# Kernel tuning notes

Measured on AMD Instinct MI355X. Metric: run time of the kernel, lower is better.

The kernel has to match this reference:

```python
import jax, jax.numpy as jnp
import numpy as np

B, H, W, C = 2, 64, 64, 320
GROUPS, EPS = 16, 1e-3  # keras GroupNormalization defaults (C>16 -> groups=16)


def quick_gelu(x):
    return x * jax.nn.sigmoid(x * 1.702)


def group_norm(x, gamma, beta):
    b, h, w, c = x.shape
    xg = x.reshape(b, h, w, GROUPS, c // GROUPS)
    mean = xg.mean(axis=(1, 2, 4), keepdims=True)
    var = xg.var(axis=(1, 2, 4), keepdims=True)
    xg = (xg - mean) * jax.lax.rsqrt(var + EPS)
    return xg.reshape(b, h, w, c) * gamma + beta


def attention(q_in, kv_in, wq, bq, wk, bk, wv, bv, wp, bp):
    # q_in, kv_in: [B,H,W,C]
    b, h, w, c = q_in.shape
    n = h * w
    scale = jnp.asarray(c, q_in.dtype) ** -0.5
    q = (q_in @ wq + bq).reshape(b, n, c)
    k = (kv_in @ wk + bk).reshape(b, n, c)
    v = (kv_in @ wv + bv).reshape(b, n, c)
    s = jax.nn.softmax(jnp.einsum('bnc,bmc->bnm', q, k) * scale, axis=-1)  # [B,N,N]
    o = jnp.einsum('bnm,bmc->bnc', s, v).reshape(b, h, w, c)
    return o @ wp + bp


def setup_inputs() -> dict:
    key = jax.random.key(0)
    ks = jax.random.split(key, 16)
    d = {
        'x': jax.random.normal(ks[0], (B, H, W, C), jnp.float32),
        'context': jax.random.normal(ks[1], (B, H, W, C), jnp.float32),
    }
    names = ['sa_q_w', 'sa_k_w', 'sa_v_w', 'sa_p_w', 'ca_q_w', 'ca_k_w', 'ca_v_w', 'ca_p_w']
    for i, nm in enumerate(names):
        d[nm] = jax.random.normal(ks[2 + i], (C, C), jnp.float32) * 0.02
        d[nm.replace('_w', '_b')] = jnp.zeros((C,), jnp.float32)
    d['ca_norm_g'] = jnp.ones((C,), jnp.float32)
    d['ca_norm_b'] = jnp.zeros((C,), jnp.float32)
    d['geglu_w'] = jax.random.normal(ks[10], (C, 8 * C), jnp.float32) * 0.02  # Conv2D 1x1 -> dense
    d['geglu_b'] = jnp.zeros((8 * C,), jnp.float32)
    d['dense_w'] = jax.random.normal(ks[11], (4 * C, C), jnp.float32) * 0.02
    d['dense_b'] = jnp.zeros((C,), jnp.float32)
    return d


def reference(x, context, sa_q_w, sa_q_b, sa_k_w, sa_k_b, sa_v_w, sa_v_b, sa_p_w, sa_p_b,
              ca_q_w, ca_q_b, ca_k_w, ca_k_b, ca_v_w, ca_v_b, ca_p_w, ca_p_b,
              ca_norm_g, ca_norm_b, geglu_w, geglu_b, dense_w, dense_b):
    # attn1: self-attention (note: its norm is defined but unused in the original call())
    a1 = x + attention(x, x, sa_q_w, sa_q_b, sa_k_w, sa_k_b, sa_v_w, sa_v_b, sa_p_w, sa_p_b)
    x = a1 + x
    # attn2: cross-attention; norm applied to query input, residual uses normalized input
    xn = group_norm(x, ca_norm_g, ca_norm_b)
    a2 = xn + attention(xn, context, ca_q_w, ca_q_b, ca_k_w, ca_k_b, ca_v_w, ca_v_b, ca_p_w, ca_p_b)
    x = a2 + x
    # GEGLU FFN (1x1 convs == dense over channels)
    xp = x @ geglu_w + geglu_b  # [B,H,W,8C]
    hdim = 4 * x.shape[-1]
    ff = xp[..., :hdim] * quick_gelu(xp[..., hdim:])
    return ff @ dense_w + dense_b + x
```

## Files before the change

kernel.cpp:

```cpp
#include <hip/hip_runtime.h>
#include <math.h>
#include <stdint.h>


typedef unsigned short u16;
typedef __attribute__((ext_vector_type(8))) short bf16x8;
typedef __attribute__((ext_vector_type(8))) unsigned short u16x8;
typedef __attribute__((ext_vector_type(4))) float f32x4;

constexpr int Bb = 2, Cc = 320;
constexpr int Nn = 64 * 64;
constexpr int Mm = Bb * Nn;
constexpr int GROUPS = 16, CG = Cc / GROUPS;
constexpr float EPS = 1e-3f;
constexpr int GN_SPLIT = 8;
constexpr int KVS = 4;
constexpr int KVC = Nn / KVS;
constexpr int KVT = 32;

__device__ __forceinline__ u16 f2b(float f) {
  unsigned u = __float_as_uint(f);
  unsigned r = u + 0x7fffu + ((u >> 16) & 1u);
  return (u16)(r >> 16);
}
__device__ __forceinline__ float b2f(u16 h) {
  return __uint_as_float(((unsigned)h) << 16);
}

template <bool F32OUT, bool DUAL>
__global__ __launch_bounds__(256) void gemm_nt(
    const u16* __restrict__ A, int lda, long long aZ,
    const u16* __restrict__ B, int ldb, long long bZ,
    const float* __restrict__ bias,
    const float* __restrict__ R1, float alpha1,
    const float* __restrict__ R2,
    void* __restrict__ Cp, int ldc, long long cZ,
    u16* __restrict__ C2,
    int K, float scale) {
  const int z = blockIdx.z;
  A += (long long)z * aZ;
  B += (long long)z * bZ;
  const long long coffz = (long long)z * cZ;

  __shared__ __align__(16) u16 As[128][40];
  __shared__ __align__(16) u16 Bs[64][40];

  const int tid = threadIdx.x;
  const int bm = blockIdx.y * 128, bn = blockIdx.x * 64;
  const int lane = tid & 63;
  const int wid = tid >> 6;
  const int wm = (wid >> 1) * 64, wn = (wid & 1) * 32;
  const int lr = lane & 15, lk = (lane >> 4) * 8;

  const int sr = tid >> 2;
  const int sk = (tid & 3) * 8;

  f32x4 acc[4][2] = {};

  const u16* Ap0 = A + (size_t)(bm + sr) * lda + sk;
  const u16* Ap1 = A + (size_t)(bm + 64 + sr) * lda + sk;
  const u16* Bp0 = B + (size_t)(bn + sr) * ldb + sk;

  for (int k0 = 0; k0 < K; k0 += 32) {
    *reinterpret_cast<u16x8*>(&As[sr][sk]) =
        *reinterpret_cast<const u16x8*>(Ap0 + k0);
    *reinterpret_cast<u16x8*>(&As[64 + sr][sk]) =
        *reinterpret_cast<const u16x8*>(Ap1 + k0);
    *reinterpret_cast<u16x8*>(&Bs[sr][sk]) =
        *reinterpret_cast<const u16x8*>(Bp0 + k0);
    __syncthreads();

    bf16x8 af[4], bfr[2];
#pragma unroll
    for (int i = 0; i < 4; ++i)
      af[i] = *reinterpret_cast<const bf16x8*>(&As[wm + i * 16 + lr][lk]);
#pragma unroll
    for (int j = 0; j < 2; ++j)
      bfr[j] = *reinterpret_cast<const bf16x8*>(&Bs[wn + j * 16 + lr][lk]);
#pragma unroll
    for (int i = 0; i < 4; ++i)
#pragma unroll
      for (int j = 0; j < 2; ++j)
        acc[i][j] = __builtin_amdgcn_mfma_f32_16x16x32_bf16(af[i], bfr[j],
                                                            acc[i][j], 0, 0, 0);
    __syncthreads();
  }

  float* Cf = (float*)Cp;
  u16* Cb = (u16*)Cp;
#pragma unroll
  for (int i = 0; i < 4; ++i)
#pragma unroll
    for (int j = 0; j < 2; ++j)
#pragma unroll
      for (int r = 0; r < 4; ++r) {
        const int row = bm + wm + i * 16 + (lane >> 4) * 4 + r;
        const int col = bn + wn + j * 16 + lr;
        const long long off = (long long)row * ldc + col + coffz;
        float v = acc[i][j][r] * scale;
        if (bias) v += bias[col];
        if (R1) v += alpha1 * R1[off];
        if (R2) v += R2[off];
        if (F32OUT) Cf[off] = v; else Cb[off] = f2b(v);
        if (DUAL) C2[off] = f2b(v);
      }
}

__global__ __launch_bounds__(256, 2) void flash_k(
    const u16* __restrict__ qb, const u16* __restrict__ kb,
    const u16* __restrict__ vtb, float* __restrict__ pO,
    float* __restrict__ pml, float scale) {
  const int qt = blockIdx.x, s = blockIdx.y, b = blockIdx.z;
  const int tid = threadIdx.x, wave = tid >> 6, lane = tid & 63;
  const int lr = lane & 15, hi = lane >> 4;
  const int qrow = qt * 64 + wave * 16;

  __shared__ __align__(16) u16 Ks[KVT][336];
  __shared__ __align__(16) u16 Vts[Cc][40];
  __shared__ __align__(16) u16 plds[4][16][72];

  bf16x8 qreg[10];
  const long long qbase = ((long long)b * Nn + qrow + lr) * Cc;
#pragma unroll
  for (int ks = 0; ks < 10; ++ks)
    qreg[ks] = *reinterpret_cast<const bf16x8*>(qb + qbase + ks * 32 + hi * 8);

  f32x4 accO[20] = {};
  float m[4] = {-INFINITY, -INFINITY, -INFINITY, -INFINITY};
  float l[4] = {0.f, 0.f, 0.f, 0.f};

  const u16* kbb = kb + (long long)b * Nn * Cc;
  const u16* vtbb = vtb + (long long)b * Cc * Nn;
  const int kv0 = s * KVC;

  const int krow = tid >> 3;
  const int kcb  = tid & 7;
  for (int t = 0; t < KVC / KVT; ++t) {
    const int kvb = kv0 + t * KVT;
    u16x8 kst[5], vst[5];
#pragma unroll
    for (int c = 0; c < 5; ++c)
      kst[c] = *reinterpret_cast<const u16x8*>(
          kbb + (long long)(kvb + krow) * Cc + (kcb + 8 * c) * 8);
#pragma unroll
    for (int c = 0; c < 5; ++c) {
      const int id = tid + 256 * c;
      const int vr = id >> 2, vc = id & 3;
      vst[c] = *reinterpret_cast<const u16x8*>(
          vtbb + (long long)vr * Nn + kvb + vc * 8);
    }
    __syncthreads();
#pragma unroll
    for (int c = 0; c < 5; ++c)
      *reinterpret_cast<u16x8*>(&Ks[krow][(kcb + 8 * c) * 8]) = kst[c];
#pragma unroll
    for (int c = 0; c < 5; ++c) {
      const int id = tid + 256 * c;
      const int vr = id >> 2, vc = id & 3;
      *reinterpret_cast<u16x8*>(&Vts[vr][vc * 8]) = vst[c];
    }
    __syncthreads();

    f32x4 accS[2] = {};
#pragma unroll
    for (int ks = 0; ks < 10; ++ks) {
#pragma unroll
      for (int j = 0; j < 2; ++j) {
        const bf16x8 bv =
            *reinterpret_cast<const bf16x8*>(&Ks[j * 16 + lr][ks * 32 + hi * 8]);
        accS[j] =
            __builtin_amdgcn_mfma_f32_16x16x32_bf16(qreg[ks], bv, accS[j], 0, 0, 0);
      }
    }
#pragma unroll
    for (int j = 0; j < 2; ++j)
#pragma unroll
      for (int r = 0; r < 4; ++r) accS[j][r] *= scale;

    float resc[4];
#pragma unroll
    for (int r = 0; r < 4; ++r) {
      float tm = fmaxf(accS[0][r], accS[1][r]);
#pragma unroll
      for (int off = 1; off < 16; off <<= 1) tm = fmaxf(tm, __shfl_xor(tm, off, 64));
      const float mn = fmaxf(m[r], tm);
      resc[r] = __expf(m[r] - mn);
      m[r] = mn;
      float ps = 0.f;
#pragma unroll
      for (int j = 0; j < 2; ++j) {
        const float p = __expf(accS[j][r] - mn);
        accS[j][r] = p;
        ps += p;
      }
#pragma unroll
      for (int off = 1; off < 16; off <<= 1) ps += __shfl_xor(ps, off, 64);
      l[r] = l[r] * resc[r] + ps;
    }
#pragma unroll
    for (int n = 0; n < 20; ++n)
#pragma unroll
      for (int r = 0; r < 4; ++r) accO[n][r] *= resc[r];

#pragma unroll
    for (int j = 0; j < 2; ++j)
#pragma unroll
      for (int r = 0; r < 4; ++r)
        plds[wave][hi * 4 + r][j * 16 + lr] = f2b(accS[j][r]);

    {
      const bf16x8 pa = *reinterpret_cast<const bf16x8*>(&plds[wave][lr][hi * 8]);
#pragma unroll
      for (int n = 0; n < 20; ++n) {
        const bf16x8 bv =
            *reinterpret_cast<const bf16x8*>(&Vts[n * 16 + lr][hi * 8]);
        accO[n] = __builtin_amdgcn_mfma_f32_16x16x32_bf16(pa, bv, accO[n], 0, 0, 0);
      }
    }
  }

  const long long obase = (((long long)(s * Bb + b)) * Nn + qrow) * Cc;
#pragma unroll
  for (int n = 0; n < 20; ++n)
#pragma unroll
    for (int r = 0; r < 4; ++r)
      pO[obase + (long long)(hi * 4 + r) * Cc + n * 16 + lr] = accO[n][r];
  if (lr == 0) {
#pragma unroll
    for (int r = 0; r < 4; ++r) {
      const long long mlb =
          (((long long)(s * Bb + b)) * Nn + qrow + hi * 4 + r) * 2;
      pml[mlb] = m[r];
      pml[mlb + 1] = l[r];
    }
  }
}

__global__ __launch_bounds__(256) void fcomb(const float* __restrict__ pO,
                                             const float* __restrict__ pml,
                                             u16* __restrict__ ob) {
  const int row = blockIdx.x * 8 + (threadIdx.x >> 5);
  const int lane32 = threadIdx.x & 31;
  const int b = row >> 12, rb = row & 4095;
  float ms[KVS], ls[KVS], mm = -INFINITY;
#pragma unroll
  for (int s = 0; s < KVS; ++s) {
    const long long i = (((long long)(s * Bb + b)) * Nn + rb) * 2;
    ms[s] = pml[i];
    ls[s] = pml[i + 1];
    mm = fmaxf(mm, ms[s]);
  }
  float w[KVS], den = 0.f;
#pragma unroll
  for (int s = 0; s < KVS; ++s) {
    w[s] = __expf(ms[s] - mm);
    den += w[s] * ls[s];
  }
  const float inv = 1.0f / den;
#pragma unroll
  for (int k = 0; k < 3; ++k) {
    const int c = k * 128 + lane32 * 4;
    if (c < Cc) {
      float4 o = {0.f, 0.f, 0.f, 0.f};
#pragma unroll
      for (int s = 0; s < KVS; ++s) {
        const float4 v = *reinterpret_cast<const float4*>(
            pO + (((long long)(s * Bb + b)) * Nn + rb) * Cc + c);
        o.x += w[s] * v.x;
        o.y += w[s] * v.y;
        o.z += w[s] * v.z;
        o.w += w[s] * v.w;
      }
      ushort4 u;
      u.x = f2b(o.x * inv);
      u.y = f2b(o.y * inv);
      u.z = f2b(o.z * inv);
      u.w = f2b(o.w * inv);
      *reinterpret_cast<ushort4*>(ob + (long long)row * Cc + c) = u;
    }
  }
}

__global__ __launch_bounds__(256) void cast_b(const float* __restrict__ in,
                                              u16* __restrict__ out) {
  const size_t i = ((size_t)blockIdx.x * 256 + threadIdx.x) * 4;
  const float4 v = *reinterpret_cast<const float4*>(in + i);
  ushort4 o;
  o.x = f2b(v.x); o.y = f2b(v.y); o.z = f2b(v.z); o.w = f2b(v.w);
  *reinterpret_cast<ushort4*>(out + i) = o;
}

__global__ __launch_bounds__(256) void tran_f2b(const float* __restrict__ in,
                                                u16* __restrict__ out, int R,
                                                int C, long long inZ,
                                                long long outZ) {
  in += (long long)blockIdx.z * inZ;
  out += (long long)blockIdx.z * outZ;
  __shared__ u16 t[32][33];
  const int c0 = blockIdx.x * 32, r0 = blockIdx.y * 32;
  const int tx = threadIdx.x, ty = threadIdx.y;
#pragma unroll
  for (int i = 0; i < 32; i += 8)
    t[ty + i][tx] = f2b(in[(size_t)(r0 + ty + i) * C + c0 + tx]);
  __syncthreads();
#pragma unroll
  for (int i = 0; i < 32; i += 8)
    out[(size_t)(c0 + ty + i) * R + r0 + tx] = t[tx][ty + i];
}

__global__ __launch_bounds__(256) void gn_stats(const float* __restrict__ x,
                                                float* __restrict__ partials) {
  const int s = blockIdx.x % GN_SPLIT;
  const int bg = blockIdx.x / GN_SPLIT;
  const int b = bg / GROUPS, g = bg % GROUPS;
  const int rows = Nn / GN_SPLIT;
  const float* base = x + (size_t)b * Nn * Cc + g * CG;
  float sum = 0.f, sq = 0.f;
  for (int i = threadIdx.x; i < rows * CG; i += 256) {
    const int r = i / CG, c = i % CG;
    const float v = base[(size_t)(s * rows + r) * Cc + c];
    sum += v; sq += v * v;
  }
#pragma unroll
  for (int off = 32; off >= 1; off >>= 1) {
    sum += __shfl_xor(sum, off, 64);
    sq += __shfl_xor(sq, off, 64);
  }
  __shared__ float rs[4], rq[4];
  const int tid = threadIdx.x;
  if ((tid & 63) == 0) { rs[tid >> 6] = sum; rq[tid >> 6] = sq; }
  __syncthreads();
  if (tid == 0) {
    partials[(bg * GN_SPLIT + s) * 2 + 0] = rs[0] + rs[1] + rs[2] + rs[3];
    partials[(bg * GN_SPLIT + s) * 2 + 1] = rq[0] + rq[1] + rq[2] + rq[3];
  }
}

__global__ __launch_bounds__(256) void gn_apply(
    const float* __restrict__ x, const float* __restrict__ partials,
    const float* __restrict__ gamma, const float* __restrict__ beta,
    float* __restrict__ xn, u16* __restrict__ xnb) {
  const size_t idx = (size_t)blockIdx.x * 256 + threadIdx.x;
  const int c = (int)(idx % Cc);
  const size_t row = idx / Cc;
  const int b = (int)(row / Nn);
  const int bg = b * GROUPS + c / CG;
  float sum = 0.f, sq = 0.f;
#pragma unroll
  for (int s = 0; s < GN_SPLIT; ++s) {
    sum += partials[(bg * GN_SPLIT + s) * 2 + 0];
    sq += partials[(bg * GN_SPLIT + s) * 2 + 1];
  }
  const float cnt = (float)Nn * CG;
  const float mean = sum / cnt;
  const float var = sq / cnt - mean * mean;
  const float r = rsqrtf(var + EPS);
  const float v = (x[idx] - mean) * r * gamma[c] + beta[c];
  xn[idx] = v;
  xnb[idx] = f2b(v);
}

__global__ __launch_bounds__(256) void geglu_comb(const u16* __restrict__ g1,
                                                  const u16* __restrict__ g2,
                                                  u16* __restrict__ ff) {
  const size_t i = ((size_t)blockIdx.x * 256 + threadIdx.x) * 4;
  const ushort4 a = *reinterpret_cast<const ushort4*>(g1 + i);
  const ushort4 b = *reinterpret_cast<const ushort4*>(g2 + i);
  ushort4 o;
  float v1, v2;
  v1 = b2f(a.x); v2 = b2f(b.x);
  o.x = f2b(v1 * (v2 / (1.0f + __expf(-1.702f * v2))));
  v1 = b2f(a.y); v2 = b2f(b.y);
  o.y = f2b(v1 * (v2 / (1.0f + __expf(-1.702f * v2))));
  v1 = b2f(a.z); v2 = b2f(b.z);
  o.z = f2b(v1 * (v2 / (1.0f + __expf(-1.702f * v2))));
  v1 = b2f(a.w); v2 = b2f(b.w);
  o.w = f2b(v1 * (v2 / (1.0f + __expf(-1.702f * v2))));
  *reinterpret_cast<ushort4*>(ff + i) = o;
}

extern "C" void kernel_launch(void* const* d_in, const int* in_sizes, int n_in,
                              void* d_out, int out_size, void* d_ws,
                              size_t ws_size, hipStream_t stream) {
  const float* x   = (const float*)d_in[0];
  const float* ctx = (const float*)d_in[1];
  const float* W[8];
  const float* Bv[8];
  for (int i = 0; i < 8; ++i) {
    W[i]  = (const float*)d_in[2 + 2 * i];
    Bv[i] = (const float*)d_in[3 + 2 * i];
  }
  const float* gn_g = (const float*)d_in[18];
  const float* gn_b = (const float*)d_in[19];
  const float* gw   = (const float*)d_in[20];
  const float* gb   = (const float*)d_in[21];
  const float* dw   = (const float*)d_in[22];
  const float* db   = (const float*)d_in[23];
  float* out = (float*)d_out;

  char* base = (char*)d_ws;
  size_t o = 0;
  auto alloc = [&](size_t bytes) {
    void* p = base + o;
    o = (o + bytes + 255) & ~(size_t)255;
    return p;
  };
  u16* wT[8];
  for (int i = 0; i < 8; ++i) wT[i] = (u16*)alloc(320 * 320 * 2);
  u16* gwT  = (u16*)alloc((size_t)2560 * 320 * 2);
  u16* dwT  = (u16*)alloc((size_t)320 * 1280 * 2);
  u16* xb   = (u16*)alloc((size_t)Mm * Cc * 2);
  u16* ctxb = (u16*)alloc((size_t)Mm * Cc * 2);
  float* x2 = (float*)alloc((size_t)Mm * Cc * 4);
  float* xn = (float*)alloc((size_t)Mm * Cc * 4);
  u16* xnb  = (u16*)alloc((size_t)Mm * Cc * 2);
  float* x3 = (float*)alloc((size_t)Mm * Cc * 4);
  u16* x3b  = (u16*)alloc((size_t)Mm * Cc * 2);
  float* stats = (float*)alloc(4096);
  const size_t SCRSZ = (size_t)20971520 + (size_t)KVS * Bb * Nn * Cc * 4 + 1048576;
  char* SCR = (char*)alloc(SCRSZ);
  u16* qb   = (u16*)SCR;
  u16* kb   = (u16*)(SCR + 5242880);
  u16* vtb  = (u16*)(SCR + 10485760);
  u16* ob   = (u16*)(SCR + 15728640);
  char* REST = SCR + 20971520;
  float* vf  = (float*)REST;
  float* pO  = (float*)REST;
  float* pml = (float*)(REST + (size_t)KVS * Bb * Nn * Cc * 4);
  u16* g1b = (u16*)SCR;
  u16* g2b = (u16*)(SCR + 20971520);
  u16* ffb = (u16*)(SCR + 41943040);

  if (base == nullptr || ws_size < o) return;

  const float scale = 1.0f / sqrtf((float)Cc);
  const long long NC = (long long)Nn * Cc;

  auto gemm_b = [&](const u16* A, int lda, long long aZ, const u16* B, int ldb,
                    long long bZ, const float* bias, u16* C, int ldc,
                    long long cZ, int Mr, int Nc, int K, float sc, int nz) {
    dim3 grid(Nc / 64, Mr / 128, nz);
    gemm_nt<false, false><<<grid, 256, 0, stream>>>(
        A, lda, aZ, B, ldb, bZ, bias, nullptr, 0.f, nullptr, C, ldc, cZ,
        nullptr, K, sc);
  };
  auto gemm_f = [&](const u16* A, int lda, const u16* B, int ldb,
                    const float* bias, const float* R1, float a1,
                    const float* R2, float* C, int ldc, int Mr, int Nc, int K) {
    dim3 grid(Nc / 64, Mr / 128, 1);
    gemm_nt<true, false><<<grid, 256, 0, stream>>>(
        A, lda, 0, B, ldb, 0, bias, R1, a1, R2, C, ldc, 0, nullptr, K, 1.f);
  };

  cast_b<<<(Mm * Cc) / 1024, 256, 0, stream>>>(x, xb);
  cast_b<<<(Mm * Cc) / 1024, 256, 0, stream>>>(ctx, ctxb);
  for (int i = 0; i < 8; ++i)
    tran_f2b<<<dim3(10, 10, 1), dim3(32, 8), 0, stream>>>(W[i], wT[i], 320, 320, 0, 0);
  tran_f2b<<<dim3(80, 10, 1), dim3(32, 8), 0, stream>>>(gw, gwT, 320, 2560, 0, 0);
  tran_f2b<<<dim3(10, 40, 1), dim3(32, 8), 0, stream>>>(dw, dwT, 1280, 320, 0, 0);

  auto attention = [&](const u16* qsrc, const u16* kv, int wi) {
    gemm_b(qsrc, Cc, 0, wT[wi + 0], Cc, 0, Bv[wi + 0], qb, Cc, 0, Mm, Cc, Cc, 1.f, 1);
    gemm_b(kv,   Cc, 0, wT[wi + 1], Cc, 0, Bv[wi + 1], kb, Cc, 0, Mm, Cc, Cc, 1.f, 1);
    {
      dim3 grid(Cc / 64, Mm / 128, 1);
      gemm_nt<true, false><<<grid, 256, 0, stream>>>(
          kv, Cc, 0, wT[wi + 2], Cc, 0, Bv[wi + 2], nullptr, 0.f, nullptr, vf,
          Cc, 0, nullptr, Cc, 1.f);
    }
    tran_f2b<<<dim3(Cc / 32, Nn / 32, 2), dim3(32, 8), 0, stream>>>(
        vf, vtb, Nn, Cc, NC, NC);
    flash_k<<<dim3(Nn / 64, KVS, Bb), 256, 0, stream>>>(qb, kb, vtb, pO, pml,
                                                        scale);
    fcomb<<<Mm / 8, 256, 0, stream>>>(pO, pml, ob);
  };

  attention(xb, xb, 0);
  gemm_f(ob, Cc, wT[3], Cc, Bv[3], x, 2.0f, nullptr, x2, Cc, Mm, Cc, Cc);

  gn_stats<<<Bb * GROUPS * GN_SPLIT, 256, 0, stream>>>(x2, stats);
  gn_apply<<<(Mm * Cc) / 256, 256, 0, stream>>>(x2, stats, gn_g, gn_b, xn, xnb);

  attention(xnb, ctxb, 4);
  {
    dim3 grid(Cc / 64, Mm / 128, 1);
    gemm_nt<true, true><<<grid, 256, 0, stream>>>(
        ob, Cc, 0, wT[7], Cc, 0, Bv[7], xn, 1.0f, x2, x3, Cc, 0, x3b, Cc, 1.f);
  }

  gemm_b(x3b, Cc, 0, gwT, Cc, 0, gb, g1b, 1280, 0, Mm, 1280, Cc, 1.f, 1);
  gemm_b(x3b, Cc, 0, gwT + (size_t)1280 * 320, Cc, 0, gb + 1280, g2b, 1280, 0,
         Mm, 1280, Cc, 1.f, 1);
  geglu_comb<<<(int)(((size_t)Mm * 1280) / 1024), 256, 0, stream>>>(g1b, g2b, ffb);
  gemm_f(ffb, 1280, dwT, 1280, db, x3, 1.0f, nullptr, out, Cc, Mm, Cc, 1280);
}
```

Baseline: 619.6 us.

## Swizzle K tile in LDS, lazy softmax rescale, raise flash occupancy

The flash attention kernel now stores K tiles in LDS with an XOR swizzle in place of padding, and shrinks the P staging buffer. This reduces bank conflicts and LDS footprint. The online softmax skips rescaling the output accumulators unless the running max grows by more than a threshold. Launch bounds ask for 3 blocks per CU, and s_setprio wraps the MFMA loops. The lazy rescale risks exp overflow bounds and adds register pressure under the tighter occupancy target, which may cause spills.

Result: slower. 909.0 us (+46.7%).

```diff
diff --git a/kernel.cpp b/kernel.cpp
--- a/kernel.cpp
+++ b/kernel.cpp
@@ -17,6 +17,7 @@
 constexpr int KVS = 4;
 constexpr int KVC = Nn / KVS;
 constexpr int KVT = 32;
+constexpr float THR = 8.f;
 
 __device__ __forceinline__ u16 f2b(float f) {
   unsigned u = __float_as_uint(f);
@@ -106,7 +107,7 @@
       }
 }
 
-__global__ __launch_bounds__(256, 2) void flash_k(
+__global__ __launch_bounds__(256, 3) void flash_k(
     const u16* __restrict__ qb, const u16* __restrict__ kb,
     const u16* __restrict__ vtb, float* __restrict__ pO,
     float* __restrict__ pml, float scale) {
@@ -115,9 +116,9 @@
   const int lr = lane & 15, hi = lane >> 4;
   const int qrow = qt * 64 + wave * 16;
 
-  __shared__ __align__(16) u16 Ks[KVT][336];
+  __shared__ __align__(16) u16 Ks[KVT * 320];
   __shared__ __align__(16) u16 Vts[Cc][40];
-  __shared__ __align__(16) u16 plds[4][16][72];
+  __shared__ __align__(16) u16 plds[4][16][40];
 
   bf16x8 qreg[10];
   const long long qbase = ((long long)b * Nn + qrow + lr) * Cc;
@@ -151,8 +152,10 @@
     }
     __syncthreads();
 #pragma unroll
-    for (int c = 0; c < 5; ++c)
-      *reinterpret_cast<u16x8*>(&Ks[krow][(kcb + 8 * c) * 8]) = kst[c];
+    for (int c = 0; c < 5; ++c) {
+      const int slot = (kcb + 8 * c) ^ (krow & 7);
+      *reinterpret_cast<u16x8*>(&Ks[krow * 320 + slot * 8]) = kst[c];
+    }
 #pragma unroll
     for (int c = 0; c < 5; ++c) {
       const int id = tid + 256 * c;
@@ -162,45 +165,63 @@
     __syncthreads();
 
     f32x4 accS[2] = {};
+    __builtin_amdgcn_s_setprio(1);
 #pragma unroll
     for (int ks = 0; ks < 10; ++ks) {
 #pragma unroll
       for (int j = 0; j < 2; ++j) {
+        const int row = j * 16 + lr;
+        const int slot = (ks * 4 + hi) ^ (row & 7);
         const bf16x8 bv =
-            *reinterpret_cast<const bf16x8*>(&Ks[j * 16 + lr][ks * 32 + hi * 8]);
+            *reinterpret_cast<const bf16x8*>(&Ks[row * 320 + slot * 8]);
         accS[j] =
             __builtin_amdgcn_mfma_f32_16x16x32_bf16(qreg[ks], bv, accS[j], 0, 0, 0);
       }
     }
+    __builtin_amdgcn_s_setprio(0);
+
 #pragma unroll
     for (int j = 0; j < 2; ++j)
 #pragma unroll
       for (int r = 0; r < 4; ++r) accS[j][r] *= scale;
 
-    float resc[4];
+    float tm[4];
 #pragma unroll
     for (int r = 0; r < 4; ++r) {
-      float tm = fmaxf(accS[0][r], accS[1][r]);
-#pragma unroll
-      for (int off = 1; off < 16; off <<= 1) tm = fmaxf(tm, __shfl_xor(tm, off, 64));
-      const float mn = fmaxf(m[r], tm);
-      resc[r] = __expf(m[r] - mn);
-      m[r] = mn;
+      float tv = fmaxf(accS[0][r], accS[1][r]);
+#pragma unroll
+      for (int off = 1; off < 16; off <<= 1) tv = fmaxf(tv, __shfl_xor(tv, off, 64));
+      tm[r] = tv;
+    }
+    const bool grow = (tm[0] > m[0] + THR) | (tm[1] > m[1] + THR) |
+                      (tm[2] > m[2] + THR) | (tm[3] > m[3] + THR);
+    if (__any(grow)) {
+      float resc[4];
+#pragma unroll
+      for (int r = 0; r < 4; ++r) {
+        const float mn = fmaxf(m[r], tm[r]);
+        resc[r] = __expf(m[r] - mn);
+        m[r] = mn;
+        l[r] *= resc[r];
+      }
+#pragma unroll
+      for (int n = 0; n < 20; ++n)
+#pragma unroll
+        for (int r = 0; r < 4; ++r) accO[n][r] *= resc[r];
+    }
+#pragma unroll
+    for (int r = 0; r < 4; ++r) {
       float ps = 0.f;
 #pragma unroll
       for (int j = 0; j < 2; ++j) {
-        const float p = __expf(accS[j][r] - mn);
+        const float p = __expf(accS[j][r] - m[r]);
         accS[j][r] = p;
         ps += p;
       }
 #pragma unroll
       for (int off = 1; off < 16; off <<= 1) ps += __shfl_xor(ps, off, 64);
-      l[r] = l[r] * resc[r] + ps;
-    }
-#pragma unroll
-    for (int n = 0; n < 20; ++n)
-#pragma unroll
-      for (int r = 0; r < 4; ++r) accO[n][r] *= resc[r];
+      l[r] += ps;
+    }
 
 #pragma unroll
     for (int j = 0; j < 2; ++j)
@@ -210,12 +231,14 @@
 
     {
       const bf16x8 pa = *reinterpret_cast<const bf16x8*>(&plds[wave][lr][hi * 8]);
+      __builtin_amdgcn_s_setprio(1);
 #pragma unroll
       for (int n = 0; n < 20; ++n) {
         const bf16x8 bv =
             *reinterpret_cast<const bf16x8*>(&Vts[n * 16 + lr][hi * 8]);
         accO[n] = __builtin_amdgcn_mfma_f32_16x16x32_bf16(pa, bv, accO[n], 0, 0, 0);
       }
+      __builtin_amdgcn_s_setprio(0);
     }
   }
 
```
